# Kernel optimization log

Hardware: AMD Instinct MI355X
Metric: run time of the kernel (lower is better)

## Reference

```python
import jax, jax.numpy as jnp
import numpy as np

N, N_UP, I, L, K = 32, 16, 128, 4, 16
H_S, H_D = 4 * I, 4          # single / double stream widths (512, 4)
F_LEN = 3 * H_S + 2 * H_D    # 1544


def setup_inputs() -> dict:
    key = jax.random.key(0)
    ks = jax.random.split(key, 11)
    f32 = jnp.float32
    return {
        "electron_positions": jax.random.normal(ks[0], (N, 3), f32),
        "nuclei_positions": jax.random.normal(ks[1], (I, 3), f32),
        # torch.rand-style U[0,1) params, scaled to avoid tanh saturation / det overflow
        "v_matrices": jax.random.uniform(ks[2], (L, N, F_LEN, H_S), f32) * 1e-3,
        "b_vectors": jax.random.uniform(ks[3], (L, N, H_S), f32),
        "w_matrices": jax.random.uniform(ks[4], (L, N, N, H_D, H_D), f32) * 0.1,
        "c_vectors": jax.random.uniform(ks[5], (L, N, N, H_D), f32),
        "final_weights": jax.random.uniform(ks[6], (K, N, H_S), f32) * 1e-3,
        "final_biases": jax.random.uniform(ks[7], (K, N), f32),
        "pi_weights": jax.random.uniform(ks[8], (K, N, I), f32) * 1e-2,
        "sigma_weights": jax.random.uniform(ks[9], (K, N, I), f32),
        "omega_weights": jax.random.uniform(ks[10], (K,), f32),
    }


def _fermi_layer(V, b, W, c, sh, dh):
    # sh: [N, H_S], dh: [N, N, H_D]
    g_up = jnp.mean(sh[:N_UP], axis=0)          # [H_S]
    g_dn = jnp.mean(sh[N_UP:], axis=0)          # [H_S]
    dg_up = jnp.mean(dh[:, :N_UP], axis=1)      # [N, H_D]
    dg_dn = jnp.mean(dh[:, N_UP:], axis=1)      # [N, H_D]
    f = jnp.concatenate(
        [sh,
         jnp.broadcast_to(g_up, (N, H_S)),
         jnp.broadcast_to(g_dn, (N, H_S)),
         dg_up, dg_dn], axis=1)                 # [N, F_LEN]
    so = jnp.tanh(jnp.einsum('nfo,nf->no', V, f) + b)      # per-electron matvec
    if so.shape == sh.shape:
        so = so + sh                            # residual (shapes always match here)
    # torch bmm(W[b,i,j], h[b,j]) -> out[b,i] = sum_j W[b,i,j] h[b,j]
    do = jnp.tanh(jnp.einsum('mnij,mnj->mni', W, dh) + c)
    if do.shape == dh.shape:
        do = do + dh
    return so, do


def _forward(electron_positions, nuclei_positions, v_matrices, b_vectors,
             w_matrices, c_vectors, final_weights, final_biases,
             pi_weights, sigma_weights, omega_weights):
    eN = electron_positions[:, None, :] - nuclei_positions[None, :, :]   # [N, I, 3]
    eN_norm = jnp.linalg.norm(eN, axis=-1)                               # [N, I]
    sh = jnp.concatenate([eN.reshape(N, 3 * I), eN_norm], axis=1)        # [N, 4I]
    ee = electron_positions[:, None, :] - electron_positions[None, :, :] # [N, N, 3]
    ee_norm = jnp.linalg.norm(ee, axis=-1, keepdims=True)                # [N, N, 1]
    dh = jnp.concatenate([ee, ee_norm], axis=-1)                         # [N, N, 4]

    # Source quirk: applies layers 0..L-2, then layer L-2 again; layers[-1] unused.
    for li in list(range(L - 1)) + [L - 2]:
        sh, dh = _fermi_layer(v_matrices[li], b_vectors[li],
                              w_matrices[li], c_vectors[li], sh, dh)

    # phi[k,i,j] = (w_ki . h_j + b_ki) * sum_m pi_kim * exp(-||sigma_kim * eN_jm||)
    fd = jnp.einsum('kid,jd->kij', final_weights, sh) + final_biases[:, :, None]
    # ||sigma * v|| = |sigma| * ||v||
    env_exp = jnp.exp(-jnp.abs(sigma_weights)[:, :, None, :]
                      * eN_norm[None, None, :, :])                        # [K,N,N,I]
    env = jnp.einsum('kim,kijm->kij', pi_weights, env_exp)                # [K,N,N]
    phi = fd * env
    d_up = jnp.linalg.det(phi[:, :N_UP, :N_UP])
    d_dn = jnp.linalg.det(phi[:, N_UP:, N_UP:])
    return jnp.sum(omega_weights * d_up * d_dn)


def reference(electron_positions, nuclei_positions, v_matrices, b_vectors,
              w_matrices, c_vectors, final_weights, final_biases,
              pi_weights, sigma_weights, omega_weights):
    return _forward(electron_positions, nuclei_positions, v_matrices, b_vectors,
                    w_matrices, c_vectors, final_weights, final_biases,
                    pi_weights, sigma_weights, omega_weights)
```

## Files before the change

kernel.cpp:

```cpp
#include <hip/hip_runtime.h>
#include <math.h>

#define N_E   32
#define NUP   16
#define N_I   128
#define H_S   512
#define F_LEN 1544
#define N_K   16
#define CH    16
#define CHUNK 97

#define WS_SH    0
#define WS_DH    16384
#define WS_ENN   20480
#define WS_PART  24576
#define WS_DETS  (24576 + 64*32*512)

__global__ void k_init(const float* __restrict__ ep, const float* __restrict__ nuc,
                       float* __restrict__ ws) {
    float* sh  = ws + WS_SH;
    float* dh  = ws + WS_DH;
    float* eNn = ws + WS_ENN;
    int t = threadIdx.x;
    for (int idx = t; idx < N_E * N_I; idx += 256) {
        int j = idx >> 7, m = idx & 127;
        float dx = ep[j*3+0] - nuc[m*3+0];
        float dy = ep[j*3+1] - nuc[m*3+1];
        float dz = ep[j*3+2] - nuc[m*3+2];
        float nr = sqrtf(dx*dx + dy*dy + dz*dz);
        eNn[j*N_I + m] = nr;
        sh[j*H_S + 3*m + 0] = dx;
        sh[j*H_S + 3*m + 1] = dy;
        sh[j*H_S + 3*m + 2] = dz;
        sh[j*H_S + 384 + m] = nr;
    }
    for (int idx = t; idx < N_E * N_E; idx += 256) {
        int a = idx >> 5, b = idx & 31;
        float dx = ep[a*3+0] - ep[b*3+0];
        float dy = ep[a*3+1] - ep[b*3+1];
        float dz = ep[a*3+2] - ep[b*3+2];
        float nr = sqrtf(dx*dx + dy*dy + dz*dz);
        float* d = dh + (a*N_E + b)*4;
        d[0] = dx; d[1] = dy; d[2] = dz; d[3] = nr;
    }
}

__global__ __launch_bounds__(256) void k_matvec(const float* __restrict__ V,
                                                const float* __restrict__ ws,
                                                float* __restrict__ partial, int li) {
    const float* sh = ws + WS_SH;
    const float* dh = ws + WS_DH;
    __shared__ float fv[CHUNK];
    int n = blockIdx.x, ch = blockIdx.y, half = blockIdx.z, t = threadIdx.x;
    int f0 = ch * CHUNK;
    int flen = F_LEN - f0; if (flen > CHUNK) flen = CHUNK;

    if (t < flen) {
        int fi = f0 + t;
        float v;
        if (fi < 512) {
            v = sh[n*H_S + fi];
        } else if (fi < 1024) {
            float s = 0.f; int o = fi - 512;
            #pragma unroll
            for (int m = 0; m < 16; ++m) s += sh[m*H_S + o];
            v = s * 0.0625f;
        } else if (fi < 1536) {
            float s = 0.f; int o = fi - 1024;
            #pragma unroll
            for (int m = 16; m < 32; ++m) s += sh[m*H_S + o];
            v = s * 0.0625f;
        } else if (fi < 1540) {
            int i = fi - 1536; float s = 0.f;
            #pragma unroll
            for (int j = 0; j < 16; ++j) s += dh[(n*N_E + j)*4 + i];
            v = s * 0.0625f;
        } else {
            int i = fi - 1540; float s = 0.f;
            #pragma unroll
            for (int j = 16; j < 32; ++j) s += dh[(n*N_E + j)*4 + i];
            v = s * 0.0625f;
        }
        fv[t] = v;
    }
    __syncthreads();

    int w  = t >> 6;
    int c4 = t & 63;
    const float* Vbase = V + ((size_t)(li*N_E + n)*F_LEN + f0)*H_S
                           + half*256 + c4*4;
    float a0 = 0.f, a1 = 0.f, a2 = 0.f, a3 = 0.f;
    #pragma unroll 8
    for (int r = w; r < flen; r += 4) {
        float4 wv = *reinterpret_cast<const float4*>(Vbase + (size_t)r * H_S);
        float fr = fv[r];
        a0 = fmaf(wv.x, fr, a0);
        a1 = fmaf(wv.y, fr, a1);
        a2 = fmaf(wv.z, fr, a2);
        a3 = fmaf(wv.w, fr, a3);
    }
    float4* pp = reinterpret_cast<float4*>(
        partial + (((size_t)(ch*4 + w))*N_E + n)*H_S + half*256) + c4;
    *pp = make_float4(a0, a1, a2, a3);
}

__global__ __launch_bounds__(512) void k_reduce(const float* __restrict__ partial,
                                                const float* __restrict__ bv,
                                                const float* __restrict__ Wm,
                                                const float* __restrict__ cv,
                                                float* __restrict__ ws, int li) {
    float* sh = ws + WS_SH;
    float* dh = ws + WS_DH;
    int n = blockIdx.x, t = threadIdx.x;
    float s = 0.f;
    #pragma unroll 16
    for (int sl = 0; sl < 64; ++sl)
        s += partial[((size_t)sl*N_E + n)*H_S + t];
    float ns = tanhf(s + bv[((size_t)li*N_E + n)*H_S + t]) + sh[n*H_S + t];

    float dval = 0.f; int j2 = 0, ii = 0;
    if (t < 128) {
        j2 = t >> 2; ii = t & 3;
        const float* Wp = Wm + ((((size_t)li*N_E + n)*N_E + j2)*4 + ii)*4;
        const float* dr = dh + (n*N_E + j2)*4;
        float acc = Wp[0]*dr[0] + Wp[1]*dr[1] + Wp[2]*dr[2] + Wp[3]*dr[3];
        dval = tanhf(acc + cv[(((size_t)li*N_E + n)*N_E + j2)*4 + ii]) + dr[ii];
    }
    __syncthreads();
    sh[n*H_S + t] = ns;
    if (t < 128) dh[(n*N_E + j2)*4 + ii] = dval;
}

__global__ __launch_bounds__(256) void k_envdet(const float* __restrict__ fw,
                                                const float* __restrict__ fb,
                                                const float* __restrict__ pw,
                                                const float* __restrict__ sw,
                                                const float* __restrict__ ws,
                                                float* __restrict__ dets) {
    const float* sh  = ws + WS_SH;
    const float* eNn = ws + WS_ENN;
    int b = blockIdx.x, k = b >> 1, sp = b & 1, base = sp * 16;
    int t = threadIdx.x;
    int i = base + (t >> 4);
    int j = base + (t & 15);

    const float* wv = fw + ((size_t)k*N_E + i)*H_S;
    const float* sv = sh + (size_t)j*H_S;
    float fd = 0.f;
    #pragma unroll 8
    for (int c = 0; c < H_S; c += 4) {
        float4 a  = *reinterpret_cast<const float4*>(wv + c);
        float4 bz = *reinterpret_cast<const float4*>(sv + c);
        fd += a.x*bz.x + a.y*bz.y + a.z*bz.z + a.w*bz.w;
    }
    fd += fb[k*N_E + i];

    const float* pv = pw + ((size_t)k*N_E + i)*N_I;
    const float* sg = sw + ((size_t)k*N_E + i)*N_I;
    const float* rn = eNn + (size_t)j*N_I;
    float env = 0.f;
    #pragma unroll 4
    for (int m = 0; m < N_I; ++m)
        env = fmaf(pv[m], expf(-fabsf(sg[m]) * rn[m]), env);

    __shared__ float phi[16][16];
    phi[t >> 4][t & 15] = fd * env;
    __syncthreads();

    if (t < 64) {
        int lane = t;
        int r = lane & 15;
        float a[16];
        #pragma unroll
        for (int c = 0; c < 16; ++c) a[c] = phi[r][c];
        bool used = (lane >= 16);
        float prod = 1.f;
        int sigma[16];
        #pragma unroll
        for (int p = 0; p < 16; ++p) {
            float v = used ? -1.f : fabsf(a[p]);
            int idx = lane;
            #pragma unroll
            for (int off = 32; off; off >>= 1) {
                float ov = __shfl_xor(v, off);
                int   oi = __shfl_xor(idx, off);
                if (ov > v || (ov == v && oi < idx)) { v = ov; idx = oi; }
            }
            int q = idx;
            float pvt = __shfl(a[p], q);
            prod *= pvt;
            sigma[p] = q;
            float factor = (!used && lane != q && pvt != 0.f) ? (a[p] / pvt) : 0.f;
            #pragma unroll
            for (int c = p; c < 16; ++c) {
                float pr = __shfl(a[c], q);
                a[c] -= factor * pr;
            }
            if (lane == q) used = true;
        }
        if (lane == 0) {
            int inv = 0;
            #pragma unroll
            for (int x = 0; x < 16; ++x)
                #pragma unroll
                for (int y = x + 1; y < 16; ++y) inv += (sigma[x] > sigma[y]) ? 1 : 0;
            dets[b] = prod * ((inv & 1) ? -1.f : 1.f);
        }
    }
}

__global__ void k_out(const float* __restrict__ dets, const float* __restrict__ omega,
                      float* __restrict__ out) {
    if (threadIdx.x == 0) {
        float s = 0.f;
        for (int k = 0; k < N_K; ++k)
            s += omega[k] * dets[2*k + 0] * dets[2*k + 1];
        out[0] = s;
    }
}

extern "C" void kernel_launch(void* const* d_in, const int* in_sizes, int n_in,
                              void* d_out, int out_size, void* d_ws, size_t ws_size,
                              hipStream_t stream) {
    const float* ep  = (const float*)d_in[0];
    const float* nuc = (const float*)d_in[1];
    const float* V   = (const float*)d_in[2];
    const float* bv  = (const float*)d_in[3];
    const float* Wm  = (const float*)d_in[4];
    const float* cv  = (const float*)d_in[5];
    const float* fw  = (const float*)d_in[6];
    const float* fb  = (const float*)d_in[7];
    const float* pw  = (const float*)d_in[8];
    const float* sw  = (const float*)d_in[9];
    const float* om  = (const float*)d_in[10];
    float* out = (float*)d_out;
    float* ws  = (float*)d_ws;

    float* partial = ws + WS_PART;
    float* dets    = ws + WS_DETS;

    k_init<<<dim3(1), dim3(256), 0, stream>>>(ep, nuc, ws);

    for (int a = 0; a < 4; ++a) {
        int li = (a < 3) ? a : 2;
        k_matvec<<<dim3(N_E, CH, 2), dim3(256), 0, stream>>>(V, ws, partial, li);
        k_reduce<<<dim3(N_E), dim3(512), 0, stream>>>(partial, bv, Wm, cv, ws, li);
    }

    k_envdet<<<dim3(2 * N_K), dim3(256), 0, stream>>>(fw, fb, pw, sw, ws, dets);
    k_out<<<dim3(1), dim3(64), 0, stream>>>(dets, om, out);
}
```

Baseline: 145.3 us.

## Fuse reduce into matvec via last-block atomic counter and ping-pong state buffers

Removes the separate reduce kernel by having the last of the 32 blocks per electron, found with an atomic counter, sum the partials and apply tanh plus the residual. sh/dh are double-buffered so blocks still reading the old state are not overwritten. The final output kernel is likewise folded into k_envdet with a last-block counter. This saves five kernel launches but adds threadfences and atomics, and the tail reduction runs serially on a single block per electron.

```diff
diff --git a/kernel.cpp b/kernel.cpp
--- a/kernel.cpp
+++ b/kernel.cpp
@@ -10,18 +10,23 @@
 #define CH    16
 #define CHUNK 97
 
-#define WS_SH    0
-#define WS_DH    16384
-#define WS_ENN   20480
-#define WS_PART  24576
-#define WS_DETS  (24576 + 64*32*512)
+#define WS_SH0   0
+#define WS_SH1   16384
+#define WS_DH0   32768
+#define WS_DH1   36864
+#define WS_ENN   40960
+#define WS_DETS  45056
+#define WS_CNT   45088
+#define WS_PART  45568
 
 __global__ void k_init(const float* __restrict__ ep, const float* __restrict__ nuc,
                        float* __restrict__ ws) {
-    float* sh  = ws + WS_SH;
-    float* dh  = ws + WS_DH;
+    float* sh  = ws + WS_SH0;
+    float* dh  = ws + WS_DH0;
     float* eNn = ws + WS_ENN;
+    int*   cnt = (int*)(ws + WS_CNT);
     int t = threadIdx.x;
+    if (t < 160) cnt[t] = 0;
     for (int idx = t; idx < N_E * N_I; idx += 256) {
         int j = idx >> 7, m = idx & 127;
         float dx = ep[j*3+0] - nuc[m*3+0];
@@ -45,11 +50,16 @@
     }
 }
 
-__global__ __launch_bounds__(256) void k_matvec(const float* __restrict__ V,
-                                                const float* __restrict__ ws,
-                                                float* __restrict__ partial, int li) {
-    const float* sh = ws + WS_SH;
-    const float* dh = ws + WS_DH;
+__global__ __launch_bounds__(256) void k_mv(const float* __restrict__ V,
+                                            const float* __restrict__ sh_in,
+                                            float* __restrict__ sh_out,
+                                            const float* __restrict__ dh_in,
+                                            float* __restrict__ dh_out,
+                                            const float* __restrict__ bv,
+                                            const float* __restrict__ Wm,
+                                            const float* __restrict__ cv,
+                                            float* __restrict__ partial,
+                                            int* __restrict__ cnt, int li) {
     __shared__ float fv[CHUNK];
     int n = blockIdx.x, ch = blockIdx.y, half = blockIdx.z, t = threadIdx.x;
     int f0 = ch * CHUNK;
@@ -59,26 +69,26 @@
         int fi = f0 + t;
         float v;
         if (fi < 512) {
-            v = sh[n*H_S + fi];
+            v = sh_in[n*H_S + fi];
         } else if (fi < 1024) {
             float s = 0.f; int o = fi - 512;
             #pragma unroll
-            for (int m = 0; m < 16; ++m) s += sh[m*H_S + o];
+            for (int m = 0; m < 16; ++m) s += sh_in[m*H_S + o];
             v = s * 0.0625f;
         } else if (fi < 1536) {
             float s = 0.f; int o = fi - 1024;
             #pragma unroll
-            for (int m = 16; m < 32; ++m) s += sh[m*H_S + o];
+            for (int m = 16; m < 32; ++m) s += sh_in[m*H_S + o];
             v = s * 0.0625f;
         } else if (fi < 1540) {
             int i = fi - 1536; float s = 0.f;
             #pragma unroll
-            for (int j = 0; j < 16; ++j) s += dh[(n*N_E + j)*4 + i];
+            for (int j = 0; j < 16; ++j) s += dh_in[(n*N_E + j)*4 + i];
             v = s * 0.0625f;
         } else {
             int i = fi - 1540; float s = 0.f;
             #pragma unroll
-            for (int j = 16; j < 32; ++j) s += dh[(n*N_E + j)*4 + i];
+            for (int j = 16; j < 32; ++j) s += dh_in[(n*N_E + j)*4 + i];
             v = s * 0.0625f;
         }
         fv[t] = v;
@@ -102,42 +112,47 @@
     float4* pp = reinterpret_cast<float4*>(
         partial + (((size_t)(ch*4 + w))*N_E + n)*H_S + half*256) + c4;
     *pp = make_float4(a0, a1, a2, a3);
-}
-
-__global__ __launch_bounds__(512) void k_reduce(const float* __restrict__ partial,
-                                                const float* __restrict__ bv,
-                                                const float* __restrict__ Wm,
-                                                const float* __restrict__ cv,
-                                                float* __restrict__ ws, int li) {
-    float* sh = ws + WS_SH;
-    float* dh = ws + WS_DH;
-    int n = blockIdx.x, t = threadIdx.x;
-    float s = 0.f;
-    #pragma unroll 16
-    for (int sl = 0; sl < 64; ++sl)
-        s += partial[((size_t)sl*N_E + n)*H_S + t];
-    float ns = tanhf(s + bv[((size_t)li*N_E + n)*H_S + t]) + sh[n*H_S + t];
-
-    float dval = 0.f; int j2 = 0, ii = 0;
+
+    __syncthreads();
+    __shared__ int tailFlag;
+    if (t == 0) {
+        __threadfence();
+        int old = atomicAdd(cnt + n, 1);
+        tailFlag = (old == 31) ? 1 : 0;
+    }
+    __syncthreads();
+    if (!tailFlag) return;
+    __threadfence();
+
+    #pragma unroll
+    for (int c = t; c < H_S; c += 256) {
+        float s = 0.f;
+        #pragma unroll 16
+        for (int sl = 0; sl < 64; ++sl)
+            s += partial[((size_t)sl*N_E + n)*H_S + c];
+        sh_out[n*H_S + c] = tanhf(s + bv[((size_t)li*N_E + n)*H_S + c])
+                            + sh_in[n*H_S + c];
+    }
     if (t < 128) {
-        j2 = t >> 2; ii = t & 3;
+        int j2 = t >> 2, ii = t & 3;
         const float* Wp = Wm + ((((size_t)li*N_E + n)*N_E + j2)*4 + ii)*4;
-        const float* dr = dh + (n*N_E + j2)*4;
+        const float* dr = dh_in + (n*N_E + j2)*4;
         float acc = Wp[0]*dr[0] + Wp[1]*dr[1] + Wp[2]*dr[2] + Wp[3]*dr[3];
-        dval = tanhf(acc + cv[(((size_t)li*N_E + n)*N_E + j2)*4 + ii]) + dr[ii];
-    }
-    __syncthreads();
-    sh[n*H_S + t] = ns;
-    if (t < 128) dh[(n*N_E + j2)*4 + ii] = dval;
+        dh_out[(n*N_E + j2)*4 + ii] =
+            tanhf(acc + cv[(((size_t)li*N_E + n)*N_E + j2)*4 + ii]) + dr[ii];
+    }
 }
 
 __global__ __launch_bounds__(256) void k_envdet(const float* __restrict__ fw,
                                                 const float* __restrict__ fb,
                                                 const float* __restrict__ pw,
                                                 const float* __restrict__ sw,
+                                                const float* __restrict__ omega,
                                                 const float* __restrict__ ws,
-                                                float* __restrict__ dets) {
-    const float* sh  = ws + WS_SH;
+                                                float* __restrict__ dets,
+                                                int* __restrict__ cnt,
+                                                float* __restrict__ out) {
+    const float* sh  = ws + WS_SH0;
     const float* eNn = ws + WS_ENN;
     int b = blockIdx.x, k = b >> 1, sp = b & 1, base = sp * 16;
     int t = threadIdx.x;
@@ -207,14 +222,21 @@
             dets[b] = prod * ((inv & 1) ? -1.f : 1.f);
         }
     }
-}
-
-__global__ void k_out(const float* __restrict__ dets, const float* __restrict__ omega,
-                      float* __restrict__ out) {
-    if (threadIdx.x == 0) {
+    __syncthreads();
+
+    __shared__ int tailFlag;
+    if (t == 0) {
+        __threadfence();
+        int old = atomicAdd(cnt, 1);
+        tailFlag = (old == 31) ? 1 : 0;
+    }
+    __syncthreads();
+    if (!tailFlag) return;
+    if (t == 0) {
+        __threadfence();
         float s = 0.f;
-        for (int k = 0; k < N_K; ++k)
-            s += omega[k] * dets[2*k + 0] * dets[2*k + 1];
+        for (int kk = 0; kk < N_K; ++kk)
+            s += omega[kk] * dets[2*kk + 0] * dets[2*kk + 1];
         out[0] = s;
     }
 }
@@ -236,17 +258,20 @@
     float* out = (float*)d_out;
     float* ws  = (float*)d_ws;
 
+    float* shb[2] = { ws + WS_SH0, ws + WS_SH1 };
+    float* dhb[2] = { ws + WS_DH0, ws + WS_DH1 };
     float* partial = ws + WS_PART;
     float* dets    = ws + WS_DETS;
+    int*   cnt     = (int*)(ws + WS_CNT);
 
     k_init<<<dim3(1), dim3(256), 0, stream>>>(ep, nuc, ws);
 
     for (int a = 0; a < 4; ++a) {
         int li = (a < 3) ? a : 2;
-        k_matvec<<<dim3(N_E, CH, 2), dim3(256), 0, stream>>>(V, ws, partial, li);
-        k_reduce<<<dim3(N_E), dim3(512), 0, stream>>>(partial, bv, Wm, cv, ws, li);
-    }
-
-    k_envdet<<<dim3(2 * N_K), dim3(256), 0, stream>>>(fw, fb, pw, sw, ws, dets);
-    k_out<<<dim3(1), dim3(64), 0, stream>>>(dets, om, out);
-}
+        k_mv<<<dim3(N_E, CH, 2), dim3(256), 0, stream>>>(
+            V, shb[a & 1], shb[(a + 1) & 1], dhb[a & 1], dhb[(a + 1) & 1],
+            bv, Wm, cv, partial, cnt + a * N_E, li);
+    }
+    k_envdet<<<dim3(2 * N_K), dim3(256), 0, stream>>>(
+        fw, fb, pw, sw, om, ws, dets, cnt + 128, out);
+}
```

After: 325.1 us. 2.24x slower.
